# Optimization experiments

Hardware: AMD Instinct MI355X
Metric: run time of the kernel (lower is better)

Reference implementation:

```python
import jax, jax.numpy as jnp
import numpy as np

THRESH = 1e-6
EPS = 1e-8
LN_EPS = 1e-5


def _layer(h, M, W_in, b_in, W_out, b_out, W_self, b_self, gamma, beta):
    # Normalize incoming flows per destination column: A[j,i] = M[j,i]/sum_k M[k,i]
    A = M / (jnp.sum(M, axis=0, keepdims=True) + EPS)
    mask = A > THRESH
    W = jnp.where(mask, A, 0.0)                      # thresholded edge weights [N,N]
    T = h @ W_in + b_in                              # transformed features [N,out]
    weighted_sum = jnp.einsum('ji,jd->id', W, T)     # sum over origins j per dest i
    weight_sum = jnp.sum(W, axis=0)                  # [N]
    has_edge = jnp.any(mask, axis=0)                 # dest i has >=1 incoming edge
    agg = jnp.where(has_edge[:, None],
                    weighted_sum / (weight_sum[:, None] + EPS),
                    T)
    agg = agg @ W_out + b_out                        # dropout is identity in eval
    out = agg + (h @ W_self + b_self)                # residual (dims differ -> self_transform)
    mu = jnp.mean(out, axis=-1, keepdims=True)
    var = jnp.mean(jnp.square(out - mu), axis=-1, keepdims=True)
    out = (out - mu) * jax.lax.rsqrt(var + LN_EPS) * gamma + beta
    return out


def setup_inputs() -> dict:
    key = jax.random.key(0)
    ks = jax.random.split(key, 16)
    N, D_IN, D_H, D_OUT = 8192, 256, 512, 256
    s = 0.05
    return {
        'node_features': jax.random.normal(ks[0], (N, D_IN), jnp.float32),
        'mobility_matrix': jax.random.uniform(ks[1], (N, N), jnp.float32),
        # layer 1: in -> hidden
        'W_in1': jax.random.normal(ks[2], (D_IN, D_H)) * s,
        'b_in1': jnp.zeros((D_H,)),
        'W_out1': jax.random.normal(ks[3], (D_H, D_H)) * s,
        'b_out1': jnp.zeros((D_H,)),
        'W_self1': jax.random.normal(ks[4], (D_IN, D_H)) * s,
        'b_self1': jnp.zeros((D_H,)),
        'g1': jnp.ones((D_H,)),
        'be1': jnp.zeros((D_H,)),
        # layer 2: hidden -> out
        'W_in2': jax.random.normal(ks[5], (D_H, D_OUT)) * s,
        'b_in2': jnp.zeros((D_OUT,)),
        'W_out2': jax.random.normal(ks[6], (D_OUT, D_OUT)) * s,
        'b_out2': jnp.zeros((D_OUT,)),
        'W_self2': jax.random.normal(ks[7], (D_H, D_OUT)) * s,
        'b_self2': jnp.zeros((D_OUT,)),
        'g2': jnp.ones((D_OUT,)),
        'be2': jnp.zeros((D_OUT,)),
    }


def reference(node_features, mobility_matrix,
              W_in1, b_in1, W_out1, b_out1, W_self1, b_self1, g1, be1,
              W_in2, b_in2, W_out2, b_out2, W_self2, b_self2, g2, be2):
    h = _layer(node_features, mobility_matrix,
               W_in1, b_in1, W_out1, b_out1, W_self1, b_self1, g1, be1)
    h = jax.nn.relu(h)  # inter-layer activation
    h = _layer(h, mobility_matrix,
               W_in2, b_in2, W_out2, b_out2, W_self2, b_self2, g2, be2)
    h = jax.nn.relu(h)  # final activation
    return h
```

## Files before the change

kernel.cpp:

```cpp
#include <hip/hip_runtime.h>
#include <stdint.h>

typedef short bf16x8 __attribute__((ext_vector_type(8)));
typedef short s16x4 __attribute__((ext_vector_type(4)));
typedef float f32x4 __attribute__((ext_vector_type(4)));
typedef unsigned int u32;
typedef unsigned char u8;

#define EPS_A 1e-8f
#define THR_A 1e-6f
#define NN 8192

static __device__ __forceinline__ short f2bf(float f) {
  u32 u = __float_as_uint(f);
  u = u + 0x7FFFu + ((u >> 16) & 1u);
  return (short)(u >> 16);
}
static __device__ __forceinline__ float bf2f(short s) {
  return __uint_as_float(((u32)(unsigned short)s) << 16);
}
static __device__ __forceinline__ u8 f2fp8(float v) {
  return (u8)(__builtin_amdgcn_cvt_pk_fp8_f32(v, v, 0, false) & 0xff);
}
static __device__ __forceinline__ void gld16(const void* g, void* l) {
  __builtin_amdgcn_global_load_lds(
      (const __attribute__((address_space(1))) u32*)g,
      (__attribute__((address_space(3))) u32*)l, 16, 0, 0);
}

__global__ __launch_bounds__(256) void k_prep_all(
    const float* __restrict__ Mob, const float* __restrict__ nf,
    const float* __restrict__ W_in1, const float* __restrict__ W_out1,
    const float* __restrict__ W_self1, const float* __restrict__ W_in2,
    const float* __restrict__ W_out2, const float* __restrict__ W_self2,
    const float* __restrict__ b_in1, const float* __restrict__ b_out1,
    const float* __restrict__ b_self1, const float* __restrict__ b_out2,
    const float* __restrict__ b_self2,
    u8* __restrict__ Mt8, float* __restrict__ colsum, u32* __restrict__ colmax,
    u8* __restrict__ nft8, short* __restrict__ A1cat, short* __restrict__ Win1b,
    short* __restrict__ Wout1t, short* __restrict__ Bcat1, short* __restrict__ Win2t,
    short* __restrict__ Bcat2, float* __restrict__ bias1c, float* __restrict__ bias2c)
{
  __shared__ __align__(16) u32 sbuf[256 * 17];
  int b = blockIdx.x;
  const int t = threadIdx.x;
  if (b < 4096) {
    const int i0 = (b & 31) * 256;
    const int j0 = (b >> 5) * 64;
    const int i = i0 + t;
    float s = 0.f, mx = 0.f;
    #pragma unroll 4
    for (int j4 = 0; j4 < 16; ++j4) {
      float v0 = Mob[(size_t)(j0 + j4 * 4 + 0) * NN + i];
      float v1 = Mob[(size_t)(j0 + j4 * 4 + 1) * NN + i];
      float v2 = Mob[(size_t)(j0 + j4 * 4 + 2) * NN + i];
      float v3 = Mob[(size_t)(j0 + j4 * 4 + 3) * NN + i];
      s += v0 + v1 + v2 + v3;
      mx = fmaxf(fmaxf(mx, fmaxf(v0, v1)), fmaxf(v2, v3));
      u32 pk = __builtin_amdgcn_cvt_pk_fp8_f32(v0, v1, 0, false);
      pk = __builtin_amdgcn_cvt_pk_fp8_f32(v2, v3, (int)pk, true);
      sbuf[t * 17 + j4] = pk;
    }
    atomicAdd(&colsum[i], s);
    atomicMax(&colmax[i], __float_as_uint(mx));
    __syncthreads();
    #pragma unroll
    for (int p = 0; p < 4; ++p) {
      const int r = p * 64 + (t >> 2);
      const int c = t & 3;
      const u32* src = &sbuf[r * 17 + c * 4];
      int4 w = make_int4(src[0], src[1], src[2], src[3]);
      *(int4*)&Mt8[(size_t)(i0 + r) * NN + j0 + c * 16] = w;
    }
    return;
  }
  b -= 4096;
  if (b < 512) {
    u8* tile = (u8*)sbuf;
    const int r0 = (b & 127) * 64, c0 = (b >> 7) * 64;
    #pragma unroll
    for (int p = 0; p < 16; ++p) {
      const int rr = p * 4 + (t >> 6), cc = t & 63;
      tile[rr * 68 + cc] = f2fp8(nf[(size_t)(r0 + rr) * 256 + c0 + cc]);
    }
    __syncthreads();
    #pragma unroll
    for (int q = 0; q < 16; ++q) {
      const int cc = q * 4 + (t >> 6), rr = t & 63;
      nft8[(size_t)(c0 + cc) * 8192 + r0 + rr] = tile[rr * 68 + cc];
    }
    return;
  }
  b -= 512;
  if (b < 2048) {
    const int idx = b * 256 + t;
    const float4 v = ((const float4*)nf)[idx];
    const int i = idx >> 6;
    const int c = (idx & 63) * 4;
    s16x4 o;
    o.x = f2bf(v.x); o.y = f2bf(v.y); o.z = f2bf(v.z); o.w = f2bf(v.w);
    *(s16x4*)&A1cat[(size_t)i * 512 + 256 + c] = o;
    return;
  }
  b -= 2048;
  if (b < 128) {
    const int idx = b * 256 + t;
    const float4 v = ((const float4*)W_in1)[idx];
    s16x4 o;
    o.x = f2bf(v.x); o.y = f2bf(v.y); o.z = f2bf(v.z); o.w = f2bf(v.w);
    *(s16x4*)&Win1b[idx * 4] = o;
    return;
  }
  b -= 128;
  if (b < 1024) {
    const int idx = b * 256 + t;
    const int r = idx >> 9, c = idx & 511;
    Wout1t[(size_t)c * 512 + r] = f2bf(W_out1[idx]);
    return;
  }
  b -= 1024;
  if (b < 512) {
    const int idx = b * 256 + t;
    const int r = idx >> 9, c = idx & 511;
    Bcat1[(size_t)c * 512 + 256 + r] = f2bf(W_self1[idx]);
    return;
  }
  b -= 512;
  if (b < 512) {
    const int idx = b * 256 + t;
    const int r = idx >> 8, c = idx & 255;
    Win2t[(size_t)c * 512 + r] = f2bf(W_in2[idx]);
    return;
  }
  b -= 512;
  if (b < 256) {
    const int idx = b * 256 + t;
    const int r = idx >> 8, c = idx & 255;
    Bcat2[(size_t)c * 768 + r] = f2bf(W_out2[idx]);
    return;
  }
  b -= 256;
  if (b < 512) {
    const int idx = b * 256 + t;
    const int r = idx >> 8, c = idx & 255;
    Bcat2[(size_t)c * 768 + 256 + r] = f2bf(W_self2[idx]);
    return;
  }
  b -= 512;
  if (b < 2) {
    const int n = b * 256 + t;
    float a = b_out1[n] + b_self1[n];
    for (int p = 0; p < 512; ++p) a += b_in1[p] * W_out1[(size_t)p * 512 + n];
    bias1c[n] = a;
    return;
  }
  bias2c[t] = b_out2[t] + b_self2[t];
}

__global__ __launch_bounds__(256) void k_gemm_raw_n(
    const short* __restrict__ A, const short* __restrict__ B, int K, int ldA, int ldB,
    short* __restrict__ C, int ldC)
{
  constexpr int LDP = 40;
  __shared__ __align__(16) short As[64 * LDP];
  __shared__ __align__(16) short Bs[64 * LDP];
  const int t = threadIdx.x;
  const int m0 = blockIdx.y * 64, n0 = blockIdx.x * 64;
  const int wid = t >> 6, l = t & 63;
  const int wr = wid >> 1, wc = wid & 1;
  const int lr = l & 15, lk = l >> 4;
  f32x4 acc[2][2] = {};
  const int sr = t >> 2;
  const int sc = (t & 3) * 8;
  const short* gA0 = A + (size_t)(m0 + sr) * ldA + sc;
  const short* gB0 = B + (size_t)(n0 + sr) * ldB + sc;
  for (int k0 = 0; k0 < K; k0 += 32) {
    const int4 a0 = *(const int4*)(gA0 + k0);
    const int4 b0 = *(const int4*)(gB0 + k0);
    __syncthreads();
    *(int4*)&As[sr * LDP + sc] = a0;
    *(int4*)&Bs[sr * LDP + sc] = b0;
    __syncthreads();
    bf16x8 av[2], bv[2];
    #pragma unroll
    for (int mi = 0; mi < 2; ++mi)
      av[mi] = *(const bf16x8*)&As[(wr * 32 + mi * 16 + lr) * LDP + lk * 8];
    #pragma unroll
    for (int ni = 0; ni < 2; ++ni)
      bv[ni] = *(const bf16x8*)&Bs[(wc * 32 + ni * 16 + lr) * LDP + lk * 8];
    #pragma unroll
    for (int mi = 0; mi < 2; ++mi)
      #pragma unroll
      for (int ni = 0; ni < 2; ++ni)
        acc[mi][ni] = __builtin_amdgcn_mfma_f32_16x16x32_bf16(av[mi], bv[ni], acc[mi][ni], 0, 0, 0);
  }
  #pragma unroll
  for (int mi = 0; mi < 2; ++mi)
    #pragma unroll
    for (int r = 0; r < 4; ++r) {
      const int m = m0 + wr * 32 + mi * 16 + lk * 4 + r;
      #pragma unroll
      for (int ni = 0; ni < 2; ++ni) {
        const int n = n0 + wc * 32 + ni * 16 + lr;
        C[(size_t)m * ldC + n] = f2bf(acc[mi][ni][r]);
      }
    }
}

template <int BN, int EPI>
__global__ __launch_bounds__(256) void k_g64(
    const short* __restrict__ A, const short* __restrict__ B, int K, int ldA, int ldB,
    void* __restrict__ Cout, int ldC, const float* __restrict__ bias0,
    u8* __restrict__ C8)
{
  constexpr int ROWS = 64 + BN;
  constexpr int CH = ROWS / 32;
  constexpr int NI = BN / 32;
  __shared__ __align__(16) short S[ROWS * 64];
  const int t = threadIdx.x;

  const int gx = gridDim.x;
  int flat = blockIdx.y * gx + blockIdx.x;
  const int cpx = (gx * gridDim.y) >> 3;
  flat = (flat & 7) * cpx + (flat >> 3);
  const int bx = flat % gx, by = flat / gx;
  const int m0 = by * 64, n0 = bx * BN;

  const int wid = t >> 6, l = t & 63;
  const int wr = wid >> 1, wc = wid & 1;
  const int lr = l & 15, lk = l >> 4;

  f32x4 acc[2][NI] = {};

  const int lrow = l >> 3, lcol = l & 7;
  const int wbase = wid * (ROWS / 4);
  short* dbase = S + wbase * 64;
  const short* gsrc[CH];
  #pragma unroll
  for (int c = 0; c < CH; ++c) {
    const int ar = wbase + c * 8 + lrow;
    const int scol = (lcol ^ (ar & 7)) * 8;
    gsrc[c] = (ar < 64) ? A + (size_t)(m0 + ar) * ldA + scol
                        : B + (size_t)(n0 + ar - 64) * ldB + scol;
  }

  const int niters = K >> 6;
  int kk = flat % niters;
  for (int it = 0; it < niters; ++it) {
    const int koff = kk << 6;
    kk = (kk + 1 == niters) ? 0 : kk + 1;
    __syncthreads();
    #pragma unroll
    for (int c = 0; c < CH; ++c)
      gld16(gsrc[c] + koff, dbase + c * 512);
    __syncthreads();

    __builtin_amdgcn_s_setprio(1);
    #pragma unroll
    for (int ks = 0; ks < 2; ++ks) {
      bf16x8 av[2], bv[NI];
      #pragma unroll
      for (int mi = 0; mi < 2; ++mi) {
        const int row = wr * 32 + mi * 16 + lr;
        av[mi] = *(const bf16x8*)&S[row * 64 + ((ks * 4 + lk) ^ (row & 7)) * 8];
      }
      #pragma unroll
      for (int ni = 0; ni < NI; ++ni) {
        const int row = 64 + wc * (BN / 2) + ni * 16 + lr;
        bv[ni] = *(const bf16x8*)&S[row * 64 + ((ks * 4 + lk) ^ (row & 7)) * 8];
      }
      #pragma unroll
      for (int mi = 0; mi < 2; ++mi)
        #pragma unroll
        for (int ni = 0; ni < NI; ++ni)
          acc[mi][ni] = __builtin_amdgcn_mfma_f32_16x16x32_bf16(av[mi], bv[ni], acc[mi][ni], 0, 0, 0);
    }
    __builtin_amdgcn_s_setprio(0);
  }

  #pragma unroll
  for (int mi = 0; mi < 2; ++mi) {
    #pragma unroll
    for (int r = 0; r < 4; ++r) {
      const int m = m0 + wr * 32 + mi * 16 + lk * 4 + r;
      float bm = 0.f;
      if (EPI == 0 || EPI == 4) bm = bias0[m];
      #pragma unroll
      for (int ni = 0; ni < NI; ++ni) {
        const int n = n0 + wc * (BN / 2) + ni * 16 + lr;
        float v = acc[mi][ni][r];
        if (EPI == 0 || EPI == 4) {
          v += bm;
          ((short*)Cout)[(size_t)m * ldC + n] = f2bf(v);
          if (EPI == 4) C8[(size_t)m * ldC + n] = f2fp8(v);
        } else {
          ((float*)Cout)[(size_t)m * ldC + n] = v + bias0[n];
        }
      }
    }
  }
}

__global__ __launch_bounds__(256) void k_sk128_f8(
    const u8* __restrict__ A, const u8* __restrict__ B, int K, int ldA, int ldB,
    short* __restrict__ P, int ldC, size_t pstride)
{
  __shared__ __align__(16) u8 S[2][16384];
  const int t = threadIdx.x;

  const int sk = blockIdx.z;
  A += (size_t)sk * K;
  B += (size_t)sk * K;

  const int gx = gridDim.x;
  int flat = blockIdx.y * gx + blockIdx.x;
  const int cpx = (gx * gridDim.y) >> 3;
  flat = (flat & 7) * cpx + (flat >> 3);
  const int bx = flat % gx, by = flat / gx;
  const int m0 = by * 128, n0 = bx * 128;

  const int wid = t >> 6, l = t & 63;
  const int wr = wid >> 1, wc = wid & 1;
  const int lr = l & 15, lk = l >> 4;

  f32x4 acc[4][4] = {};

  const int side = wid >> 1;
  const int hrow = (wid & 1) * 64;
  const u8* Xp = side ? B : A;
  const int ldX = side ? ldB : ldA;
  const int x0 = side ? n0 : m0;
  const int doff = side * 8192 + hrow * 64;
  u8* d0 = &S[0][doff];
  u8* d1 = &S[1][doff];
  const u8* gsrc[4];
  #pragma unroll
  for (int c = 0; c < 4; ++c) {
    const int row = hrow + c * 16 + (l >> 2);
    const int ql = (l & 3) ^ (row & 3);
    gsrc[c] = Xp + (size_t)(x0 + row) * ldX + ql * 16;
  }

  const int niters = K >> 6;
  int kk = (flat + sk * 3) & (niters - 1);
  {
    const int koff = kk << 6;
    kk = (kk + 1) & (niters - 1);
    gld16(gsrc[0] + koff, d0);
    gld16(gsrc[1] + koff, d0 + 1024);
    gld16(gsrc[2] + koff, d0 + 2048);
    gld16(gsrc[3] + koff, d0 + 3072);
  }

  int buf = 0;
  for (int it = 0; it < niters; ++it) {
    if (it + 1 < niters) {
      const int koff = kk << 6;
      kk = (kk + 1) & (niters - 1);
      u8* nb = buf ? d0 : d1;
      gld16(gsrc[0] + koff, nb);
      gld16(gsrc[1] + koff, nb + 1024);
      gld16(gsrc[2] + koff, nb + 2048);
      gld16(gsrc[3] + koff, nb + 3072);
      asm volatile("s_waitcnt vmcnt(4)" ::: "memory");
    } else {
      asm volatile("s_waitcnt vmcnt(0)" ::: "memory");
    }
    __builtin_amdgcn_sched_barrier(0);
    __builtin_amdgcn_s_barrier();

    const u8* Ab = &S[buf][0];
    const u8* Bb = &S[buf][8192];
    __builtin_amdgcn_s_setprio(1);
    #pragma unroll
    for (int ks = 0; ks < 2; ++ks) {
      const int q = ks * 2 + (lk >> 1);
      const int inner = (lk & 1) * 8;
      long av[4], bv[4];
      #pragma unroll
      for (int mi = 0; mi < 4; ++mi) {
        const int row = wr * 64 + mi * 16 + lr;
        av[mi] = *(const long*)&Ab[row * 64 + ((q ^ (row & 3)) << 4) + inner];
      }
      #pragma unroll
      for (int ni = 0; ni < 4; ++ni) {
        const int row = wc * 64 + ni * 16 + lr;
        bv[ni] = *(const long*)&Bb[row * 64 + ((q ^ (row & 3)) << 4) + inner];
      }
      #pragma unroll
      for (int mi = 0; mi < 4; ++mi)
        #pragma unroll
        for (int ni = 0; ni < 4; ++ni)
          acc[mi][ni] = __builtin_amdgcn_mfma_f32_16x16x32_fp8_fp8(av[mi], bv[ni], acc[mi][ni], 0, 0, 0);
    }
    __builtin_amdgcn_s_setprio(0);
    __builtin_amdgcn_s_barrier();
    buf ^= 1;
  }

  short* outp = P + pstride * sk;
  #pragma unroll
  for (int mi = 0; mi < 4; ++mi) {
    #pragma unroll
    for (int r = 0; r < 4; ++r) {
      const int m = m0 + wr * 64 + mi * 16 + lk * 4 + r;
      #pragma unroll
      for (int ni = 0; ni < 4; ++ni) {
        const int n = n0 + wc * 64 + ni * 16 + lr;
        outp[(size_t)m * ldC + n] = f2bf(acc[mi][ni][r]);
      }
    }
  }
}

__global__ __launch_bounds__(256) void k_sk_reduce_sub(
    const short* __restrict__ P, int N, size_t pstride, int S,
    const float* __restrict__ colsum, const u32* __restrict__ colmax,
    const short* __restrict__ hraw, int ldh,
    short* __restrict__ out, int ldo)
{
  const int idx = blockIdx.x * 256 + threadIdx.x;
  const int nq = N >> 2;
  const int m = idx / nq;
  const int c4 = (idx - m * nq) * 4;
  const size_t base = (size_t)m * N + c4;
  float a0 = 0.f, a1 = 0.f, a2 = 0.f, a3 = 0.f;
  for (int s = 0; s < S; ++s) {
    s16x4 v = *(const s16x4*)&P[pstride * s + base];
    a0 += bf2f(v.x); a1 += bf2f(v.y); a2 += bf2f(v.z); a3 += bf2f(v.w);
  }
  const float cs = colsum[m];
  const float rc = 1.f / (cs + EPS_A);
  const float rcw = rc / (cs * rc + EPS_A);
  const bool he = __uint_as_float(colmax[m]) * rc > THR_A;
  s16x4 o;
  if (he) {
    o.x = f2bf(a0 * rcw); o.y = f2bf(a1 * rcw);
    o.z = f2bf(a2 * rcw); o.w = f2bf(a3 * rcw);
  } else {
    o = *(const s16x4*)&hraw[(size_t)m * ldh + c4];
  }
  *(s16x4*)&out[(size_t)m * ldo + c4] = o;
}

__global__ __launch_bounds__(256) void k_sk_reduce(
    const short* __restrict__ P, int N, size_t pstride, int S,
    const float* __restrict__ colsum, const u32* __restrict__ colmax,
    const short* __restrict__ Tfall, short* __restrict__ out, int ldo)
{
  const int idx = blockIdx.x * 256 + threadIdx.x;
  const int nq = N >> 2;
  const int m = idx / nq;
  const int c4 = (idx - m * nq) * 4;
  const size_t base = (size_t)m * N + c4;
  float a0 = 0.f, a1 = 0.f, a2 = 0.f, a3 = 0.f;
  for (int s = 0; s < S; ++s) {
    s16x4 v = *(const s16x4*)&P[pstride * s + base];
    a0 += bf2f(v.x); a1 += bf2f(v.y); a2 += bf2f(v.z); a3 += bf2f(v.w);
  }
  const float cs = colsum[m];
  const float rc = 1.f / (cs + EPS_A);
  const float rcw = rc / (cs * rc + EPS_A);
  const bool he = __uint_as_float(colmax[m]) * rc > THR_A;
  a0 *= rcw; a1 *= rcw; a2 *= rcw; a3 *= rcw;
  if (__ballot(!he)) {
    if (!he) {
      a0 = bf2f(Tfall[(size_t)(c4 + 0) * NN + m]);
      a1 = bf2f(Tfall[(size_t)(c4 + 1) * NN + m]);
      a2 = bf2f(Tfall[(size_t)(c4 + 2) * NN + m]);
      a3 = bf2f(Tfall[(size_t)(c4 + 3) * NN + m]);
    }
  }
  s16x4 o;
  o.x = f2bf(a0); o.y = f2bf(a1); o.z = f2bf(a2); o.w = f2bf(a3);
  *(s16x4*)&out[(size_t)m * ldo + c4] = o;
}

template <int MODE>
__device__ __forceinline__ void ln_relu_body(
    const float* __restrict__ X, int W,
    const float* __restrict__ g, const float* __restrict__ be,
    void* __restrict__ out, int ldo)
{
  const int row = blockIdx.x;
  const int t = threadIdx.x;
  const float* x = X + (size_t)row * W;
  float v0 = x[t], v1 = 0.f;
  float s = v0, ss = v0 * v0;
  if (W == 512) { v1 = x[t + 256]; s += v1; ss += v1 * v1; }
  #pragma unroll
  for (int off = 32; off; off >>= 1) {
    s += __shfl_down(s, off);
    ss += __shfl_down(ss, off);
  }
  __shared__ float red[8];
  const int wid = t >> 6;
  if ((t & 63) == 0) { red[wid] = s; red[4 + wid] = ss; }
  __syncthreads();
  s = red[0] + red[1] + red[2] + red[3];
  ss = red[4] + red[5] + red[6] + red[7];
  const float mu = s / W;
  const float var = ss / W - mu * mu;
  const float sc = rsqrtf(var + 1e-5f);
  float y = fmaxf((v0 - mu) * sc * g[t] + be[t], 0.f);
  if (MODE == 0) ((short*)out)[(size_t)row * ldo + t] = f2bf(y);
  else           ((float*)out)[(size_t)row * ldo + t] = y;
  if (W == 512) {
    float y1 = fmaxf((v1 - mu) * sc * g[t + 256] + be[t + 256], 0.f);
    if (MODE == 0) ((short*)out)[(size_t)row * ldo + t + 256] = f2bf(y1);
    else           ((float*)out)[(size_t)row * ldo + t + 256] = y1;
  }
}

__global__ __launch_bounds__(256) void k_ln_relu_bf16(
    const float* __restrict__ X, int W, const float* __restrict__ g,
    const float* __restrict__ be, short* __restrict__ out, int ldo) {
  ln_relu_body<0>(X, W, g, be, out, ldo);
}
__global__ __launch_bounds__(256) void k_ln_relu_f32(
    const float* __restrict__ X, int W, const float* __restrict__ g,
    const float* __restrict__ be, float* __restrict__ out, int ldo) {
  ln_relu_body<1>(X, W, g, be, out, ldo);
}

extern "C" void kernel_launch(void* const* d_in, const int* in_sizes, int n_in,
                              void* d_out, int out_size, void* d_ws, size_t ws_size,
                              hipStream_t stream) {
  const float* nf      = (const float*)d_in[0];
  const float* Mob     = (const float*)d_in[1];
  const float* W_in1   = (const float*)d_in[2];
  const float* b_in1   = (const float*)d_in[3];
  const float* W_out1  = (const float*)d_in[4];
  const float* b_out1  = (const float*)d_in[5];
  const float* W_self1 = (const float*)d_in[6];
  const float* b_self1 = (const float*)d_in[7];
  const float* g1      = (const float*)d_in[8];
  const float* be1     = (const float*)d_in[9];
  const float* W_in2   = (const float*)d_in[10];
  const float* b_in2   = (const float*)d_in[11];
  const float* W_out2  = (const float*)d_in[12];
  const float* b_out2  = (const float*)d_in[13];
  const float* W_self2 = (const float*)d_in[14];
  const float* b_self2 = (const float*)d_in[15];
  const float* g2      = (const float*)d_in[16];
  const float* be2     = (const float*)d_in[17];

  char* ws = (char*)d_ws;
  float* colsum = (float*)(ws);
  u32*   colmax = (u32*)(ws + 32768);
  u8*    Mt8    = (u8*)(ws + 131072);
  u8*    nft8   = (u8*)(ws + 67239936);
  u8*    T2t8   = (u8*)(ws + 69337088);
  short* A1cat  = (short*)(ws + 71434240);
  float* C2f    = (float*)(ws + 79822848);
  short* Acat2  = (short*)(ws + 96600064);
  short* T2t    = (short*)(ws + 109182976);
  short* Bcat1  = (short*)(ws + 113377280);
  short* Bcat2  = (short*)(ws + 113901568);
  short* Win2t  = (short*)(ws + 114294784);
  short* Wout1t = (short*)(ws + 114556928);
  short* Win1b  = (short*)(ws + 115081216);
  float* bias1c = (float*)(ws + 115343360);
  float* bias2c = (float*)(ws + 115345408);
  short* P1     = (short*)(ws + 117440512);
  short* P2     = (short*)(ws + 150994944);

  hipMemsetAsync(ws, 0, 65536, stream);

  k_prep_all<<<9603, 256, 0, stream>>>(Mob, nf, W_in1, W_out1, W_self1, W_in2,
                                       W_out2, W_self2, b_in1, b_out1, b_self1,
                                       b_out2, b_self2, Mt8, colsum, colmax, nft8,
                                       A1cat, Win1b, Wout1t, Bcat1, Win2t, Bcat2,
                                       bias1c, bias2c);
  k_gemm_raw_n<<<dim3(4, 8), 256, 0, stream>>>(Wout1t, Win1b, 512, 512, 512,
                                               Bcat1, 512);

  k_sk128_f8<<<dim3(2, 64, 8), 256, 0, stream>>>(Mt8, nft8, 1024, NN, NN,
                                                 P1, 256, (size_t)8192 * 256);
  k_sk_reduce_sub<<<2048, 256, 0, stream>>>(P1, 256, (size_t)8192 * 256, 8,
                                            colsum, colmax, A1cat + 256, 512,
                                            A1cat, 512);
  k_g64<128, 2><<<dim3(4, 128), 256, 0, stream>>>(A1cat, Bcat1, 512, 512, 512,
                                                  C2f, 512, bias1c, nullptr);
  k_ln_relu_bf16<<<8192, 256, 0, stream>>>(C2f, 512, g1, be1, Acat2 + 256, 768);

  k_g64<64, 4><<<dim3(128, 4), 256, 0, stream>>>(Win2t, Acat2 + 256, 512, 512, 768,
                                                 T2t, NN, b_in2, T2t8);
  k_sk128_f8<<<dim3(2, 64, 8), 256, 0, stream>>>(Mt8, T2t8, 1024, NN, NN,
                                                 P2, 256, (size_t)8192 * 256);
  k_sk_reduce<<<2048, 256, 0, stream>>>(P2, 256, (size_t)8192 * 256, 8,
                                        colsum, colmax, T2t, Acat2, 768);
  k_g64<64, 2><<<dim3(4, 128), 256, 0, stream>>>(Acat2, Bcat2, 768, 768, 768,
                                                 C2f, 256, bias2c, nullptr);
  k_ln_relu_f32<<<8192, 256, 0, stream>>>(C2f, 256, g2, be2, (float*)d_out, 256);
}
```

Baseline: 266.1 us.

## Double-buffer LDS tiles in k_g64 to overlap global loads with MFMA

Converts the single-buffered shared-memory tile in the k_g64 GEMM into a ping-pong pair, issuing the next K-tile's global-to-LDS loads before computing on the current one. Partial vmcnt waits replace the two full __syncthreads per iteration, so load latency can hide behind MFMA work. LDS use doubles, which may reduce occupancy, and correctness depends on the hand-written vmcnt counts matching the number of loads issued per chunk.

```diff
diff --git a/kernel.cpp b/kernel.cpp
--- a/kernel.cpp
+++ b/kernel.cpp
@@ -216,7 +216,7 @@
   constexpr int ROWS = 64 + BN;
   constexpr int CH = ROWS / 32;
   constexpr int NI = BN / 32;
-  __shared__ __align__(16) short S[ROWS * 64];
+  __shared__ __align__(16) short S[2][ROWS * 64];
   const int t = threadIdx.x;
 
   const int gx = gridDim.x;
@@ -234,7 +234,8 @@
 
   const int lrow = l >> 3, lcol = l & 7;
   const int wbase = wid * (ROWS / 4);
-  short* dbase = S + wbase * 64;
+  short* d0 = &S[0][wbase * 64];
+  short* d1 = &S[1][wbase * 64];
   const short* gsrc[CH];
   #pragma unroll
   for (int c = 0; c < CH; ++c) {
@@ -246,15 +247,34 @@
 
   const int niters = K >> 6;
   int kk = flat % niters;
-  for (int it = 0; it < niters; ++it) {
+  {
     const int koff = kk << 6;
     kk = (kk + 1 == niters) ? 0 : kk + 1;
-    __syncthreads();
     #pragma unroll
     for (int c = 0; c < CH; ++c)
-      gld16(gsrc[c] + koff, dbase + c * 512);
-    __syncthreads();
-
+      gld16(gsrc[c] + koff, d0 + c * 512);
+  }
+
+  int buf = 0;
+  for (int it = 0; it < niters; ++it) {
+    if (it + 1 < niters) {
+      const int koff = kk << 6;
+      kk = (kk + 1 == niters) ? 0 : kk + 1;
+      short* nb = buf ? d0 : d1;
+      #pragma unroll
+      for (int c = 0; c < CH; ++c)
+        gld16(gsrc[c] + koff, nb + c * 512);
+      if constexpr (CH == 6)
+        asm volatile("s_waitcnt vmcnt(6)" ::: "memory");
+      else
+        asm volatile("s_waitcnt vmcnt(4)" ::: "memory");
+    } else {
+      asm volatile("s_waitcnt vmcnt(0)" ::: "memory");
+    }
+    __builtin_amdgcn_sched_barrier(0);
+    __builtin_amdgcn_s_barrier();
+
+    const short* Sb = S[buf];
     __builtin_amdgcn_s_setprio(1);
     #pragma unroll
     for (int ks = 0; ks < 2; ++ks) {
@@ -262,12 +282,12 @@
       #pragma unroll
       for (int mi = 0; mi < 2; ++mi) {
         const int row = wr * 32 + mi * 16 + lr;
-        av[mi] = *(const bf16x8*)&S[row * 64 + ((ks * 4 + lk) ^ (row & 7)) * 8];
+        av[mi] = *(const bf16x8*)&Sb[row * 64 + ((ks * 4 + lk) ^ (row & 7)) * 8];
       }
       #pragma unroll
       for (int ni = 0; ni < NI; ++ni) {
         const int row = 64 + wc * (BN / 2) + ni * 16 + lr;
-        bv[ni] = *(const bf16x8*)&S[row * 64 + ((ks * 4 + lk) ^ (row & 7)) * 8];
+        bv[ni] = *(const bf16x8*)&Sb[row * 64 + ((ks * 4 + lk) ^ (row & 7)) * 8];
       }
       #pragma unroll
       for (int mi = 0; mi < 2; ++mi)
@@ -276,6 +296,8 @@
           acc[mi][ni] = __builtin_amdgcn_mfma_f32_16x16x32_bf16(av[mi], bv[ni], acc[mi][ni], 0, 0, 0);
     }
     __builtin_amdgcn_s_setprio(0);
+    __builtin_amdgcn_s_barrier();
+    buf ^= 1;
   }
 
   #pragma unroll
```

After: 263.3 us. No clear change (-1.0%).
